# Kernel optimization log

Hardware: AMD Instinct MI355X
Metric: run time of the kernel (lower is better)

Reference implementation:

```python
import jax, jax.numpy as jnp
import numpy as np

N_NODES = 100000
N_EDGES = 3200000


def gcn_conv(x, row, col, W, n):
    # PyG GCNConv: x @ W, then D^{-1/2}(A+I)D^{-1/2} aggregation (self-loops added).
    h = x @ W  # [N, out]
    loop = jnp.arange(n)
    r = jnp.concatenate([row, loop])
    c = jnp.concatenate([col, loop])
    deg = jax.ops.segment_sum(jnp.ones_like(c, dtype=h.dtype), c, num_segments=n)
    dinv = jnp.where(deg > 0, jax.lax.rsqrt(deg), 0.0)
    norm = dinv[r] * dinv[c]  # [E+N]
    msg = h[r] * norm[:, None]  # gather + scale
    return jax.ops.segment_sum(msg, c, num_segments=n)  # scatter-add


def setup_inputs() -> dict:
    key = jax.random.key(0)
    k1, k2, k3, k4, k5 = jax.random.split(key, 5)
    x = jax.random.normal(k1, (N_NODES, 1), dtype=jnp.float32)
    edge_index = jax.random.randint(k2, (2, N_EDGES), 0, N_NODES, dtype=jnp.int64)
    W1 = jax.random.normal(k3, (1, 16), dtype=jnp.float32) * 0.5
    W2 = jax.random.normal(k4, (16, 16), dtype=jnp.float32) * 0.25
    W3 = jax.random.normal(k5, (16, 11), dtype=jnp.float32) * 0.25
    b = jnp.zeros((11,), dtype=jnp.float32)
    return {"x": x, "edge_index": edge_index, "W1": W1, "W2": W2, "W3": W3, "b": b}


def reference(x, edge_index, W1, W2, W3, b):
    n = x.shape[0]
    row, col = edge_index[0], edge_index[1]
    h = jax.nn.relu(gcn_conv(x, row, col, W1, n))
    h = jax.nn.relu(gcn_conv(h, row, col, W2, n))
    g = jnp.mean(h, axis=0).reshape(-1, 16)  # [1,16] graph readout
    out = (g @ W3).squeeze() + b  # [11]
    return out
```

## Files before the change

kernel.cpp:

```cpp
#include <hip/hip_runtime.h>

static constexpr int N = 100000;
static constexpr int E = 3200000;
static constexpr int BUKSHIFT = 8;
static constexpr int BUKSZ = 1 << BUKSHIFT;
static constexpr int BUKMASK = BUKSZ - 1;
static constexpr int NBUK = (N + BUKSZ - 1) / BUKSZ;
static constexpr int NGRP = 8;
static constexpr int SUBCAP = 1536;
static constexpr int CAP = NGRP * SUBCAP;
static constexpr int GSTRIDE = 16;
static constexpr int SC_CHUNK = 4096;
static constexpr int SC_T = 512;
static constexpr int SC_BLOCKS = (E + SC_CHUNK - 1) / SC_CHUNK;


__global__ void k_init(int* __restrict__ gofs) {
    int i = blockIdx.x * blockDim.x + threadIdx.x;
    if (i < NBUK * NGRP) gofs[i * GSTRIDE] = 0;
}

__global__ __launch_bounds__(SC_T) void k_scatter(const int4* __restrict__ rows4,
                                                  const int4* __restrict__ cols4,
                                                  int* __restrict__ gofs,
                                                  int* __restrict__ binned) {
    __shared__ int hist[2 * NBUK];
    __shared__ int cnt[512];
    __shared__ int lbase[NBUK];
    __shared__ int gbase[NBUK];
    __shared__ int stag[SC_CHUNK];

    const int tid = threadIdx.x;
    const int g = tid >> 8;
    const int grp = blockIdx.x & (NGRP - 1);
    for (int i = tid; i < 2 * NBUK; i += SC_T) hist[i] = 0;
    cnt[tid] = 0;
    __syncthreads();

    const int nI4 = E / 4;
    const int base4 = blockIdx.x * (SC_CHUNK / 4);
    const int ia = base4 + tid, ib = base4 + SC_T + tid;
    const bool va = ia < nI4, vb = ib < nI4;
    int4 ra, ca, rb, cb;
    if (va) { ra = rows4[ia]; ca = cols4[ia]; }
    if (vb) { rb = rows4[ib]; cb = cols4[ib]; }

    if (va) {
        atomicAdd(&hist[g * NBUK + (ca.x >> BUKSHIFT)], 1);
        atomicAdd(&hist[g * NBUK + (ca.y >> BUKSHIFT)], 1);
        atomicAdd(&hist[g * NBUK + (ca.z >> BUKSHIFT)], 1);
        atomicAdd(&hist[g * NBUK + (ca.w >> BUKSHIFT)], 1);
    }
    if (vb) {
        atomicAdd(&hist[g * NBUK + (cb.x >> BUKSHIFT)], 1);
        atomicAdd(&hist[g * NBUK + (cb.y >> BUKSHIFT)], 1);
        atomicAdd(&hist[g * NBUK + (cb.z >> BUKSHIFT)], 1);
        atomicAdd(&hist[g * NBUK + (cb.w >> BUKSHIFT)], 1);
    }
    __syncthreads();

    if (tid < NBUK) {
        int h0 = hist[0 * NBUK + tid], h1 = hist[1 * NBUK + tid];
        hist[0 * NBUK + tid] = 0;
        hist[1 * NBUK + tid] = h0;
        int c = h0 + h1;
        cnt[tid] = c;
        int off = c ? atomicAdd(&gofs[(tid * NGRP + grp) * GSTRIDE], c) : 0;
        gbase[tid] = tid * CAP + grp * SUBCAP + off;
    }
    __syncthreads();
    for (int off = 1; off < 512; off <<= 1) {
        int v = cnt[tid];
        if (tid >= off) v += cnt[tid - off];
        __syncthreads();
        cnt[tid] = v;
        __syncthreads();
    }
    if (tid < NBUK) lbase[tid] = tid ? cnt[tid - 1] : 0;
    __syncthreads();

    if (va) {
        int b, off;
        b = ca.x >> BUKSHIFT; off = atomicAdd(&hist[g * NBUK + b], 1); stag[lbase[b] + off] = (ra.x << BUKSHIFT) | (ca.x & BUKMASK);
        b = ca.y >> BUKSHIFT; off = atomicAdd(&hist[g * NBUK + b], 1); stag[lbase[b] + off] = (ra.y << BUKSHIFT) | (ca.y & BUKMASK);
        b = ca.z >> BUKSHIFT; off = atomicAdd(&hist[g * NBUK + b], 1); stag[lbase[b] + off] = (ra.z << BUKSHIFT) | (ca.z & BUKMASK);
        b = ca.w >> BUKSHIFT; off = atomicAdd(&hist[g * NBUK + b], 1); stag[lbase[b] + off] = (ra.w << BUKSHIFT) | (ca.w & BUKMASK);
    }
    if (vb) {
        int b, off;
        b = cb.x >> BUKSHIFT; off = atomicAdd(&hist[g * NBUK + b], 1); stag[lbase[b] + off] = (rb.x << BUKSHIFT) | (cb.x & BUKMASK);
        b = cb.y >> BUKSHIFT; off = atomicAdd(&hist[g * NBUK + b], 1); stag[lbase[b] + off] = (rb.y << BUKSHIFT) | (cb.y & BUKMASK);
        b = cb.z >> BUKSHIFT; off = atomicAdd(&hist[g * NBUK + b], 1); stag[lbase[b] + off] = (rb.z << BUKSHIFT) | (cb.z & BUKMASK);
        b = cb.w >> BUKSHIFT; off = atomicAdd(&hist[g * NBUK + b], 1); stag[lbase[b] + off] = (rb.w << BUKSHIFT) | (cb.w & BUKMASK);
    }
    __syncthreads();

    const int eTot = min(SC_CHUNK, E - blockIdx.x * SC_CHUNK);
    int s = tid * 8;
    if (s < eTot) {
        int lo = 0, hi = NBUK - 1;
        while (lo < hi) { int mid = (lo + hi + 1) >> 1; if (lbase[mid] <= s) lo = mid; else hi = mid - 1; }
        int b = lo;
        const int e1 = min(s + 8, eTot);
        for (; s < e1; ++s) {
            while (b + 1 < NBUK && lbase[b + 1] <= s) ++b;
            binned[gbase[b] + (s - lbase[b])] = stag[s];
        }
    }
}

__global__ __launch_bounds__(1024) void k_deg(const int* __restrict__ binned,
                                              const int* __restrict__ gofs,
                                              const float* __restrict__ x,
                                              float* __restrict__ dinv,
                                              float* __restrict__ y1) {
    __shared__ int cnt[8][BUKSZ];
    const int tid = threadIdx.x;
    for (int i = tid; i < 8 * BUKSZ; i += 1024) (&cnt[0][0])[i] = 0;
    __syncthreads();
    const int b = blockIdx.x, g = tid >> 7;
    for (int sg = 0; sg < NGRP; ++sg) {
        const int s0 = b * CAP + sg * SUBCAP;
        const int n = gofs[(b * NGRP + sg) * GSTRIDE];
        const int n4 = n >> 2;
        const int4* b4 = (const int4*)(binned + s0);
        for (int i = tid; i < n4; i += 1024) {
            int4 p = b4[i];
            atomicAdd(&cnt[g][p.x & BUKMASK], 1);
            atomicAdd(&cnt[g][p.y & BUKMASK], 1);
            atomicAdd(&cnt[g][p.z & BUKMASK], 1);
            atomicAdd(&cnt[g][p.w & BUKMASK], 1);
        }
        if (tid < (n & 3)) atomicAdd(&cnt[g][binned[s0 + (n4 << 2) + tid] & BUKMASK], 1);
    }
    __syncthreads();
    if (tid < BUKSZ) {
        int v = (b << BUKSHIFT) + tid;
        if (v < N) {
            int c = 0;
            #pragma unroll
            for (int q = 0; q < 8; ++q) c += cnt[q][tid];
            float d = rsqrtf(1.0f + (float)c);
            dinv[v] = d;
            y1[v] = d * x[v];
        }
    }
}

__global__ __launch_bounds__(1024) void k_acc1(const int* __restrict__ binned,
                                               const int* __restrict__ gofs,
                                               const float* __restrict__ y1,
                                               const float* __restrict__ dinv,
                                               float* __restrict__ m) {
    __shared__ float acc[8][BUKSZ];
    const int tid = threadIdx.x;
    for (int i = tid; i < 8 * BUKSZ; i += 1024) (&acc[0][0])[i] = 0.f;
    __syncthreads();
    const int b = blockIdx.x, g = tid >> 7;
    for (int sg = 0; sg < NGRP; ++sg) {
        const int s0 = b * CAP + sg * SUBCAP;
        const int n = gofs[(b * NGRP + sg) * GSTRIDE];
        const int n4 = n >> 2;
        const int4* b4 = (const int4*)(binned + s0);
        for (int i = tid; i < n4; i += 1024) {
            int4 p = b4[i];
            atomicAdd(&acc[g][p.x & BUKMASK], y1[p.x >> BUKSHIFT]);
            atomicAdd(&acc[g][p.y & BUKMASK], y1[p.y >> BUKSHIFT]);
            atomicAdd(&acc[g][p.z & BUKMASK], y1[p.z >> BUKSHIFT]);
            atomicAdd(&acc[g][p.w & BUKMASK], y1[p.w >> BUKSHIFT]);
        }
        if (tid < (n & 3)) {
            int p = binned[s0 + (n4 << 2) + tid];
            atomicAdd(&acc[g][p & BUKMASK], y1[p >> BUKSHIFT]);
        }
    }
    __syncthreads();
    if (tid < BUKSZ) {
        int v = (b << BUKSHIFT) + tid;
        if (v < N) {
            float a = 0.f;
            #pragma unroll
            for (int q = 0; q < 8; ++q) a += acc[q][tid];
            float d = dinv[v];
            float s = d * a + d * y1[v];
            m[v] = d * s;
        }
    }
}

__global__ __launch_bounds__(1024) void k_acc2(const int* __restrict__ binned,
                                               const int* __restrict__ gofs,
                                               const float* __restrict__ m,
                                               const float* __restrict__ dinv,
                                               const float* __restrict__ W1,
                                               const float* __restrict__ W2,
                                               float* __restrict__ partials) {
    __shared__ float tp[8][BUKSZ], tn[8][BUKSZ];
    __shared__ float sP[16], sM[16], sAcc[16];
    const int tid = threadIdx.x;
    if (tid < 16) {
        float p = 0.f, q = 0.f;
        for (int k = 0; k < 16; ++k) {
            float w1 = W1[k];
            float w2 = W2[k * 16 + tid];
            p += fmaxf(w1, 0.f) * w2;
            q += fminf(w1, 0.f) * w2;
        }
        sP[tid] = p; sM[tid] = q; sAcc[tid] = 0.f;
    }
    for (int i = tid; i < 8 * BUKSZ; i += 1024) { (&tp[0][0])[i] = 0.f; (&tn[0][0])[i] = 0.f; }
    __syncthreads();
    const int b = blockIdx.x, g = tid >> 7;
    for (int sg = 0; sg < NGRP; ++sg) {
        const int s0 = b * CAP + sg * SUBCAP;
        const int n = gofs[(b * NGRP + sg) * GSTRIDE];
        const int n4 = n >> 2;
        const int4* b4 = (const int4*)(binned + s0);
        for (int i = tid; i < n4; i += 1024) {
            int4 p = b4[i];
            float v0 = m[p.x >> BUKSHIFT], v1 = m[p.y >> BUKSHIFT];
            float v2 = m[p.z >> BUKSHIFT], v3 = m[p.w >> BUKSHIFT];
            atomicAdd(v0 >= 0.f ? &tp[g][p.x & BUKMASK] : &tn[g][p.x & BUKMASK], v0);
            atomicAdd(v1 >= 0.f ? &tp[g][p.y & BUKMASK] : &tn[g][p.y & BUKMASK], v1);
            atomicAdd(v2 >= 0.f ? &tp[g][p.z & BUKMASK] : &tn[g][p.z & BUKMASK], v2);
            atomicAdd(v3 >= 0.f ? &tp[g][p.w & BUKMASK] : &tn[g][p.w & BUKMASK], v3);
        }
        if (tid < (n & 3)) {
            int p = binned[s0 + (n4 << 2) + tid];
            float val = m[p >> BUKSHIFT];
            atomicAdd(val >= 0.f ? &tp[g][p & BUKMASK] : &tn[g][p & BUKMASK], val);
        }
    }
    __syncthreads();
    float alpha = 0.f, beta = 0.f;
    if (tid < BUKSZ) {
        int v = (b << BUKSHIFT) + tid;
        if (v < N) {
            float a = 0.f, bb = 0.f;
            #pragma unroll
            for (int q = 0; q < 8; ++q) { a += tp[q][tid]; bb += tn[q][tid]; }
            float d = dinv[v], mv = m[v];
            alpha = d * a;
            beta  = d * bb;
            float self = d * mv;
            if (mv >= 0.f) alpha += self; else beta += self;
        }
    }
    const int lane = tid & 63;
    for (int j = 0; j < 16; ++j) {
        float h = fmaxf(alpha * sP[j] + beta * sM[j], 0.f);
        #pragma unroll
        for (int off = 32; off > 0; off >>= 1) h += __shfl_down(h, off);
        if (lane == 0 && h != 0.f) atomicAdd(&sAcc[j], h);
    }
    __syncthreads();
    if (tid < 16) partials[b * 16 + tid] = sAcc[tid];
}

__global__ void k_out(const float* __restrict__ partials, const float* __restrict__ W3,
                      const float* __restrict__ b, float* __restrict__ out) {
    __shared__ float s[16][16];
    int j = threadIdx.x & 15;
    int g = threadIdx.x >> 4;
    float acc = 0.f;
    for (int blk = g; blk < NBUK; blk += 16) acc += partials[blk * 16 + j];
    s[g][j] = acc;
    __syncthreads();
    if (threadIdx.x < 16) {
        float tot = 0.f;
        #pragma unroll
        for (int gg = 0; gg < 16; ++gg) tot += s[gg][threadIdx.x];
        s[0][threadIdx.x] = tot * (1.0f / (float)N);
    }
    __syncthreads();
    if (threadIdx.x < 11) {
        float acc2 = b[threadIdx.x];
        #pragma unroll
        for (int k = 0; k < 16; ++k) acc2 += s[0][k] * W3[k * 11 + threadIdx.x];
        out[threadIdx.x] = acc2;
    }
}

extern "C" void kernel_launch(void* const* d_in, const int* in_sizes, int n_in,
                              void* d_out, int out_size, void* d_ws, size_t ws_size,
                              hipStream_t stream) {
    const float* x  = (const float*)d_in[0];
    const int*   ei = (const int*)d_in[1];
    const float* W1 = (const float*)d_in[2];
    const float* W2 = (const float*)d_in[3];
    const float* W3 = (const float*)d_in[4];
    const float* b  = (const float*)d_in[5];
    float* out = (float*)d_out;

    int*   wsi      = (int*)d_ws;
    int*   binned   = wsi;
    float* dinv     = (float*)(wsi + (size_t)NBUK * CAP);
    float* y1       = dinv + N;
    float* m        = y1 + N;
    int*   gofs     = (int*)(m + N);
    float* partials = (float*)(gofs + NBUK * NGRP * GSTRIDE);

    const int4* rows4 = (const int4*)ei;
    const int4* cols4 = (const int4*)(ei + E);

    k_init   <<<(NBUK * NGRP + 511) / 512, 512, 0, stream>>>(gofs);
    k_scatter<<<SC_BLOCKS, SC_T, 0, stream>>>(rows4, cols4, gofs, binned);
    k_deg    <<<NBUK, 1024, 0, stream>>>(binned, gofs, x, dinv, y1);
    k_acc1   <<<NBUK, 1024, 0, stream>>>(binned, gofs, y1, dinv, m);
    k_acc2   <<<NBUK, 1024, 0, stream>>>(binned, gofs, m, dinv, W1, W2, partials);
    k_out    <<<1, 256, 0, stream>>>(partials, W3, b, out);
}
```

Before: 118.1 us.

## Drop LDS staging in scatter and use single per-bucket global cursor

```diff
diff --git a/kernel.cpp b/kernel.cpp
--- a/kernel.cpp
+++ b/kernel.cpp
@@ -6,9 +6,7 @@
 static constexpr int BUKSZ = 1 << BUKSHIFT;
 static constexpr int BUKMASK = BUKSZ - 1;
 static constexpr int NBUK = (N + BUKSZ - 1) / BUKSZ;
-static constexpr int NGRP = 8;
-static constexpr int SUBCAP = 1536;
-static constexpr int CAP = NGRP * SUBCAP;
+static constexpr int CAP = 12288;
 static constexpr int GSTRIDE = 16;
 static constexpr int SC_CHUNK = 4096;
 static constexpr int SC_T = 512;
@@ -17,24 +15,19 @@
 
 __global__ void k_init(int* __restrict__ gofs) {
     int i = blockIdx.x * blockDim.x + threadIdx.x;
-    if (i < NBUK * NGRP) gofs[i * GSTRIDE] = 0;
+    if (i < NBUK) gofs[i * GSTRIDE] = i * CAP;
 }
 
 __global__ __launch_bounds__(SC_T) void k_scatter(const int4* __restrict__ rows4,
                                                   const int4* __restrict__ cols4,
                                                   int* __restrict__ gofs,
                                                   int* __restrict__ binned) {
-    __shared__ int hist[2 * NBUK];
-    __shared__ int cnt[512];
-    __shared__ int lbase[NBUK];
+    __shared__ int hist[4 * NBUK];
     __shared__ int gbase[NBUK];
-    __shared__ int stag[SC_CHUNK];
-
-    const int tid = threadIdx.x;
-    const int g = tid >> 8;
-    const int grp = blockIdx.x & (NGRP - 1);
-    for (int i = tid; i < 2 * NBUK; i += SC_T) hist[i] = 0;
-    cnt[tid] = 0;
+
+    const int tid = threadIdx.x;
+    const int g = tid >> 7;
+    for (int i = tid; i < 4 * NBUK; i += SC_T) hist[i] = 0;
     __syncthreads();
 
     const int nI4 = E / 4;
@@ -61,51 +54,29 @@
 
     if (tid < NBUK) {
         int h0 = hist[0 * NBUK + tid], h1 = hist[1 * NBUK + tid];
+        int h2 = hist[2 * NBUK + tid], h3 = hist[3 * NBUK + tid];
         hist[0 * NBUK + tid] = 0;
         hist[1 * NBUK + tid] = h0;
-        int c = h0 + h1;
-        cnt[tid] = c;
-        int off = c ? atomicAdd(&gofs[(tid * NGRP + grp) * GSTRIDE], c) : 0;
-        gbase[tid] = tid * CAP + grp * SUBCAP + off;
-    }
-    __syncthreads();
-    for (int off = 1; off < 512; off <<= 1) {
-        int v = cnt[tid];
-        if (tid >= off) v += cnt[tid - off];
-        __syncthreads();
-        cnt[tid] = v;
-        __syncthreads();
-    }
-    if (tid < NBUK) lbase[tid] = tid ? cnt[tid - 1] : 0;
+        hist[2 * NBUK + tid] = h0 + h1;
+        hist[3 * NBUK + tid] = h0 + h1 + h2;
+        int c = h0 + h1 + h2 + h3;
+        gbase[tid] = c ? atomicAdd(&gofs[tid * GSTRIDE], c) : 0;
+    }
     __syncthreads();
 
     if (va) {
         int b, off;
-        b = ca.x >> BUKSHIFT; off = atomicAdd(&hist[g * NBUK + b], 1); stag[lbase[b] + off] = (ra.x << BUKSHIFT) | (ca.x & BUKMASK);
-        b = ca.y >> BUKSHIFT; off = atomicAdd(&hist[g * NBUK + b], 1); stag[lbase[b] + off] = (ra.y << BUKSHIFT) | (ca.y & BUKMASK);
-        b = ca.z >> BUKSHIFT; off = atomicAdd(&hist[g * NBUK + b], 1); stag[lbase[b] + off] = (ra.z << BUKSHIFT) | (ca.z & BUKMASK);
-        b = ca.w >> BUKSHIFT; off = atomicAdd(&hist[g * NBUK + b], 1); stag[lbase[b] + off] = (ra.w << BUKSHIFT) | (ca.w & BUKMASK);
+        b = ca.x >> BUKSHIFT; off = atomicAdd(&hist[g * NBUK + b], 1); binned[gbase[b] + off] = (ra.x << BUKSHIFT) | (ca.x & BUKMASK);
+        b = ca.y >> BUKSHIFT; off = atomicAdd(&hist[g * NBUK + b], 1); binned[gbase[b] + off] = (ra.y << BUKSHIFT) | (ca.y & BUKMASK);
+        b = ca.z >> BUKSHIFT; off = atomicAdd(&hist[g * NBUK + b], 1); binned[gbase[b] + off] = (ra.z << BUKSHIFT) | (ca.z & BUKMASK);
+        b = ca.w >> BUKSHIFT; off = atomicAdd(&hist[g * NBUK + b], 1); binned[gbase[b] + off] = (ra.w << BUKSHIFT) | (ca.w & BUKMASK);
     }
     if (vb) {
         int b, off;
-        b = cb.x >> BUKSHIFT; off = atomicAdd(&hist[g * NBUK + b], 1); stag[lbase[b] + off] = (rb.x << BUKSHIFT) | (cb.x & BUKMASK);
-        b = cb.y >> BUKSHIFT; off = atomicAdd(&hist[g * NBUK + b], 1); stag[lbase[b] + off] = (rb.y << BUKSHIFT) | (cb.y & BUKMASK);
-        b = cb.z >> BUKSHIFT; off = atomicAdd(&hist[g * NBUK + b], 1); stag[lbase[b] + off] = (rb.z << BUKSHIFT) | (cb.z & BUKMASK);
-        b = cb.w >> BUKSHIFT; off = atomicAdd(&hist[g * NBUK + b], 1); stag[lbase[b] + off] = (rb.w << BUKSHIFT) | (cb.w & BUKMASK);
-    }
-    __syncthreads();
-
-    const int eTot = min(SC_CHUNK, E - blockIdx.x * SC_CHUNK);
-    int s = tid * 8;
-    if (s < eTot) {
-        int lo = 0, hi = NBUK - 1;
-        while (lo < hi) { int mid = (lo + hi + 1) >> 1; if (lbase[mid] <= s) lo = mid; else hi = mid - 1; }
-        int b = lo;
-        const int e1 = min(s + 8, eTot);
-        for (; s < e1; ++s) {
-            while (b + 1 < NBUK && lbase[b + 1] <= s) ++b;
-            binned[gbase[b] + (s - lbase[b])] = stag[s];
-        }
+        b = cb.x >> BUKSHIFT; off = atomicAdd(&hist[g * NBUK + b], 1); binned[gbase[b] + off] = (rb.x << BUKSHIFT) | (cb.x & BUKMASK);
+        b = cb.y >> BUKSHIFT; off = atomicAdd(&hist[g * NBUK + b], 1); binned[gbase[b] + off] = (rb.y << BUKSHIFT) | (cb.y & BUKMASK);
+        b = cb.z >> BUKSHIFT; off = atomicAdd(&hist[g * NBUK + b], 1); binned[gbase[b] + off] = (rb.z << BUKSHIFT) | (cb.z & BUKMASK);
+        b = cb.w >> BUKSHIFT; off = atomicAdd(&hist[g * NBUK + b], 1); binned[gbase[b] + off] = (rb.w << BUKSHIFT) | (cb.w & BUKMASK);
     }
 }
 
@@ -119,20 +90,18 @@
     for (int i = tid; i < 8 * BUKSZ; i += 1024) (&cnt[0][0])[i] = 0;
     __syncthreads();
     const int b = blockIdx.x, g = tid >> 7;
-    for (int sg = 0; sg < NGRP; ++sg) {
-        const int s0 = b * CAP + sg * SUBCAP;
-        const int n = gofs[(b * NGRP + sg) * GSTRIDE];
-        const int n4 = n >> 2;
-        const int4* b4 = (const int4*)(binned + s0);
-        for (int i = tid; i < n4; i += 1024) {
-            int4 p = b4[i];
-            atomicAdd(&cnt[g][p.x & BUKMASK], 1);
-            atomicAdd(&cnt[g][p.y & BUKMASK], 1);
-            atomicAdd(&cnt[g][p.z & BUKMASK], 1);
-            atomicAdd(&cnt[g][p.w & BUKMASK], 1);
-        }
-        if (tid < (n & 3)) atomicAdd(&cnt[g][binned[s0 + (n4 << 2) + tid] & BUKMASK], 1);
-    }
+    const int s0 = b * CAP;
+    const int n = gofs[b * GSTRIDE] - s0;
+    const int n4 = n >> 2;
+    const int4* b4 = (const int4*)(binned + s0);
+    for (int i = tid; i < n4; i += 1024) {
+        int4 p = b4[i];
+        atomicAdd(&cnt[g][p.x & BUKMASK], 1);
+        atomicAdd(&cnt[g][p.y & BUKMASK], 1);
+        atomicAdd(&cnt[g][p.z & BUKMASK], 1);
+        atomicAdd(&cnt[g][p.w & BUKMASK], 1);
+    }
+    if (tid < (n & 3)) atomicAdd(&cnt[g][binned[s0 + (n4 << 2) + tid] & BUKMASK], 1);
     __syncthreads();
     if (tid < BUKSZ) {
         int v = (b << BUKSHIFT) + tid;
@@ -157,22 +126,20 @@
     for (int i = tid; i < 8 * BUKSZ; i += 1024) (&acc[0][0])[i] = 0.f;
     __syncthreads();
     const int b = blockIdx.x, g = tid >> 7;
-    for (int sg = 0; sg < NGRP; ++sg) {
-        const int s0 = b * CAP + sg * SUBCAP;
-        const int n = gofs[(b * NGRP + sg) * GSTRIDE];
-        const int n4 = n >> 2;
-        const int4* b4 = (const int4*)(binned + s0);
-        for (int i = tid; i < n4; i += 1024) {
-            int4 p = b4[i];
-            atomicAdd(&acc[g][p.x & BUKMASK], y1[p.x >> BUKSHIFT]);
-            atomicAdd(&acc[g][p.y & BUKMASK], y1[p.y >> BUKSHIFT]);
-            atomicAdd(&acc[g][p.z & BUKMASK], y1[p.z >> BUKSHIFT]);
-            atomicAdd(&acc[g][p.w & BUKMASK], y1[p.w >> BUKSHIFT]);
-        }
-        if (tid < (n & 3)) {
-            int p = binned[s0 + (n4 << 2) + tid];
-            atomicAdd(&acc[g][p & BUKMASK], y1[p >> BUKSHIFT]);
-        }
+    const int s0 = b * CAP;
+    const int n = gofs[b * GSTRIDE] - s0;
+    const int n4 = n >> 2;
+    const int4* b4 = (const int4*)(binned + s0);
+    for (int i = tid; i < n4; i += 1024) {
+        int4 p = b4[i];
+        atomicAdd(&acc[g][p.x & BUKMASK], y1[p.x >> BUKSHIFT]);
+        atomicAdd(&acc[g][p.y & BUKMASK], y1[p.y >> BUKSHIFT]);
+        atomicAdd(&acc[g][p.z & BUKMASK], y1[p.z >> BUKSHIFT]);
+        atomicAdd(&acc[g][p.w & BUKMASK], y1[p.w >> BUKSHIFT]);
+    }
+    if (tid < (n & 3)) {
+        int p = binned[s0 + (n4 << 2) + tid];
+        atomicAdd(&acc[g][p & BUKMASK], y1[p >> BUKSHIFT]);
     }
     __syncthreads();
     if (tid < BUKSZ) {
@@ -211,25 +178,23 @@
     for (int i = tid; i < 8 * BUKSZ; i += 1024) { (&tp[0][0])[i] = 0.f; (&tn[0][0])[i] = 0.f; }
     __syncthreads();
     const int b = blockIdx.x, g = tid >> 7;
-    for (int sg = 0; sg < NGRP; ++sg) {
-        const int s0 = b * CAP + sg * SUBCAP;
-        const int n = gofs[(b * NGRP + sg) * GSTRIDE];
-        const int n4 = n >> 2;
-        const int4* b4 = (const int4*)(binned + s0);
-        for (int i = tid; i < n4; i += 1024) {
-            int4 p = b4[i];
-            float v0 = m[p.x >> BUKSHIFT], v1 = m[p.y >> BUKSHIFT];
-            float v2 = m[p.z >> BUKSHIFT], v3 = m[p.w >> BUKSHIFT];
-            atomicAdd(v0 >= 0.f ? &tp[g][p.x & BUKMASK] : &tn[g][p.x & BUKMASK], v0);
-            atomicAdd(v1 >= 0.f ? &tp[g][p.y & BUKMASK] : &tn[g][p.y & BUKMASK], v1);
-            atomicAdd(v2 >= 0.f ? &tp[g][p.z & BUKMASK] : &tn[g][p.z & BUKMASK], v2);
-            atomicAdd(v3 >= 0.f ? &tp[g][p.w & BUKMASK] : &tn[g][p.w & BUKMASK], v3);
-        }
-        if (tid < (n & 3)) {
-            int p = binned[s0 + (n4 << 2) + tid];
-            float val = m[p >> BUKSHIFT];
-            atomicAdd(val >= 0.f ? &tp[g][p & BUKMASK] : &tn[g][p & BUKMASK], val);
-        }
+    const int s0 = b * CAP;
+    const int n = gofs[b * GSTRIDE] - s0;
+    const int n4 = n >> 2;
+    const int4* b4 = (const int4*)(binned + s0);
+    for (int i = tid; i < n4; i += 1024) {
+        int4 p = b4[i];
+        float v0 = m[p.x >> BUKSHIFT], v1 = m[p.y >> BUKSHIFT];
+        float v2 = m[p.z >> BUKSHIFT], v3 = m[p.w >> BUKSHIFT];
+        atomicAdd(v0 >= 0.f ? &tp[g][p.x & BUKMASK] : &tn[g][p.x & BUKMASK], v0);
+        atomicAdd(v1 >= 0.f ? &tp[g][p.y & BUKMASK] : &tn[g][p.y & BUKMASK], v1);
+        atomicAdd(v2 >= 0.f ? &tp[g][p.z & BUKMASK] : &tn[g][p.z & BUKMASK], v2);
+        atomicAdd(v3 >= 0.f ? &tp[g][p.w & BUKMASK] : &tn[g][p.w & BUKMASK], v3);
+    }
+    if (tid < (n & 3)) {
+        int p = binned[s0 + (n4 << 2) + tid];
+        float val = m[p >> BUKSHIFT];
+        atomicAdd(val >= 0.f ? &tp[g][p & BUKMASK] : &tn[g][p & BUKMASK], val);
     }
     __syncthreads();
     float alpha = 0.f, beta = 0.f;
@@ -298,12 +263,12 @@
     float* y1       = dinv + N;
     float* m        = y1 + N;
     int*   gofs     = (int*)(m + N);
-    float* partials = (float*)(gofs + NBUK * NGRP * GSTRIDE);
+    float* partials = (float*)(gofs + NBUK * GSTRIDE);
 
     const int4* rows4 = (const int4*)ei;
     const int4* cols4 = (const int4*)(ei + E);
 
-    k_init   <<<(NBUK * NGRP + 511) / 512, 512, 0, stream>>>(gofs);
+    k_init   <<<1, 512, 0, stream>>>(gofs);
     k_scatter<<<SC_BLOCKS, SC_T, 0, stream>>>(rows4, cols4, gofs, binned);
     k_deg    <<<NBUK, 1024, 0, stream>>>(binned, gofs, x, dinv, y1);
     k_acc1   <<<NBUK, 1024, 0, stream>>>(binned, gofs, y1, dinv, m);
```

New measurement: 118.0 us. No clear change (-0.1%).
